# Kernel tuning notes

Hardware: AMD Instinct MI355X
Metric: run time of the kernel (lower is better)

## Reference

```python
import jax, jax.numpy as jnp
import numpy as np
import math

NUM_CLASSES = 80
ANCHORS = [(12.0, 16.0), (19.0, 36.0), (40.0, 28.0)]
ANGLES = [-np.pi/3, -np.pi/6, 0.0, np.pi/6, np.pi/3, np.pi/2]
STRIDE = 8.0
SCALE_XY = 1.05
IGNORE_THRESH = 0.5
MASKED_ANCHORS = np.array([[w/STRIDE, h/STRIDE, a] for (w, h) in ANCHORS for a in ANGLES], dtype=np.float32)  # [18,3]
NA = MASKED_ANCHORS.shape[0]
LAMBDA_COORD, LAMBDA_CONF, LAMBDA_CLS = 1.0, 10.0, 1.0
FOCAL_ALPHA, FOCAL_GAMMA = 0.25, 2.0


def setup_inputs() -> dict:
    key = jax.random.key(0)
    B, G, nT = 8, 76, 240
    k1, k2, k3, k4, k5, k6 = jax.random.split(key, 6)
    output = jax.random.normal(k1, (B, NA * (NUM_CLASSES + 6), G, G), jnp.float32) * 0.1
    tb = jax.random.randint(k2, (nT,), 0, B).astype(jnp.float32)
    tl = jax.random.randint(k3, (nT,), 0, NUM_CLASSES).astype(jnp.float32)
    txy = jax.random.uniform(k4, (nT, 2), minval=0.02, maxval=0.98)
    twh = jax.random.uniform(k5, (nT, 2), minval=0.05, maxval=0.4)
    tang = jax.random.uniform(k6, (nT, 1), minval=-np.pi/2, maxval=np.pi/2)
    target = jnp.concatenate([tb[:, None], tl[:, None], txy, twh, tang], axis=-1)  # [nT,7]
    return {"output": output, "target": target}


def _smooth_l1(x, y):
    d = jnp.abs(x - y)
    return jnp.where(d < 1.0, 0.5 * d * d, d - 0.5)


def _bce(p, t):
    eps = 1e-7
    p = jnp.clip(p, eps, 1.0 - eps)
    return -(t * jnp.log(p) + (1.0 - t) * jnp.log(1.0 - p))


def _focal(p, t):
    loss = _bce(p, t)
    p_t = t * p + (1.0 - t) * (1.0 - p)
    alpha_f = t * FOCAL_ALPHA + (1.0 - t) * (1.0 - FOCAL_ALPHA)
    return loss * alpha_f * (1.0 - p_t) ** FOCAL_GAMMA


def _ciou(pb, tb):
    # pb, tb: [N,5] (cx, cy, w, h, angle) in grid units
    p1, p2 = pb[:, :2] - pb[:, 2:4] / 2, pb[:, :2] + pb[:, 2:4] / 2
    t1, t2 = tb[:, :2] - tb[:, 2:4] / 2, tb[:, :2] + tb[:, 2:4] / 2
    w1, h1 = p2[:, 0] - p1[:, 0], p2[:, 1] - p1[:, 1]
    w2, h2 = t2[:, 0] - t1[:, 0], t2[:, 1] - t1[:, 1]
    area1, area2 = w1 * h1, w2 * h2
    c1, c2 = (p1 + p2) / 2, (t1 + t2) / 2
    inter = jnp.clip(jnp.minimum(p2, t2) - jnp.maximum(p1, t1), 0.0)
    inter_area = inter[:, 0] * inter[:, 1]
    inter_diag = jnp.sum((c2 - c1) ** 2, axis=-1)
    outer = jnp.clip(jnp.maximum(p2, t2) - jnp.minimum(p1, t1), 0.0)
    outer_diag = outer[:, 0] ** 2 + outer[:, 1] ** 2
    union = area1 + area2 - inter_area
    u = inter_diag / outer_diag
    iou = inter_area / union
    v = (4.0 / math.pi ** 2) * (jnp.arctan(w2 / h2) - jnp.arctan(w1 / h1)) ** 2
    alpha = jax.lax.stop_gradient(v / ((1.0 - iou) + v))
    ciou = jnp.clip(iou - (u + alpha * v), -1.0, 1.0)
    skew_iou = iou * jnp.abs(jnp.cos(pb[:, 4] - tb[:, 4]))
    return skew_iou, ciou


def _forward(output, target):
    B, G = output.shape[0], output.shape[2]
    nC = NUM_CLASSES
    ma = jnp.asarray(MASKED_ANCHORS)
    pred = output.reshape(B, NA, nC + 6, G, G).transpose(0, 1, 3, 4, 2)  # [B,A,G,G,C+6]
    px = jax.nn.sigmoid(pred[..., 0]) * SCALE_XY - (SCALE_XY - 1) / 2
    py = jax.nn.sigmoid(pred[..., 1]) * SCALE_XY - (SCALE_XY - 1) / 2
    pw, ph, pa = pred[..., 2], pred[..., 3], pred[..., 4]
    pconf = jax.nn.sigmoid(pred[..., 5])
    pcls = jax.nn.sigmoid(pred[..., 6:])
    gx = jnp.arange(G, dtype=output.dtype)[None, None, None, :]
    gy = jnp.arange(G, dtype=output.dtype)[None, None, :, None]
    aw = ma[:, 0].reshape(1, NA, 1, 1)
    ah = ma[:, 1].reshape(1, NA, 1, 1)
    aa = ma[:, 2].reshape(1, NA, 1, 1)
    pred_boxes = jnp.stack([px + gx, py + gy, jnp.exp(pw) * aw, jnp.exp(ph) * ah, pa + aa], axis=-1)  # [B,A,G,G,5]
    out_dec = jnp.concatenate([
        jnp.concatenate([pred_boxes[..., :4] * STRIDE, pred_boxes[..., 4:]], axis=-1).reshape(B, -1, 5),
        pconf.reshape(B, -1, 1),
        pcls.reshape(B, -1, nC)], axis=-1)

    # ---- build_targets ----
    tgt_boxes = jnp.concatenate([target[:, 2:6] * G, target[:, 6:]], axis=-1)  # [nT,5]
    gxy, gwh, ga = tgt_boxes[:, :2], tgt_boxes[:, 2:4], tgt_boxes[:, 4]
    aw_, ah_, aa_ = ma[:, 0][:, None], ma[:, 1][:, None], ma[:, 2][:, None]  # [A,1]
    w2, h2 = gwh[:, 0][None, :], gwh[:, 1][None, :]                          # [1,nT]
    inter = jnp.minimum(aw_, w2) * jnp.minimum(ah_, h2)
    union = aw_ * ah_ + 1e-16 + w2 * h2 - inter
    offset = jnp.abs(aa_ - ga[None, :])                                       # [A,nT]
    arious = (inter / union) * jnp.abs(jnp.cos(aa_ - ga[None, :]))            # [A,nT]
    best_n = jnp.argmax(arious, axis=0)                                       # [nT]
    b = target[:, 0].astype(jnp.int32)
    labels = target[:, 1].astype(jnp.int32)
    gi = gxy[:, 0].astype(jnp.int32)
    gj = gxy[:, 1].astype(jnp.int32)

    zeros = jnp.zeros((B, NA, G, G), output.dtype)
    obj = zeros.at[b, best_n, gj, gi].set(1.0)
    noobj = jnp.ones((B, NA, G, G), output.dtype)
    cond = (arious > IGNORE_THRESH) | ((arious > 0.4) & (offset < np.pi / 12))  # [A,nT]
    a_idx = jnp.broadcast_to(jnp.arange(NA)[:, None], arious.shape)
    bb = jnp.broadcast_to(b[None, :], arious.shape)
    gjb = jnp.broadcast_to(gj[None, :], arious.shape)
    gib = jnp.broadcast_to(gi[None, :], arious.shape)
    noobj = noobj.at[bb, a_idx, gjb, gib].min(jnp.where(cond, 0.0, 1.0))
    noobj = noobj.at[b, best_n, gj, gi].set(0.0)

    ta_grid = zeros.at[b, best_n, gj, gi].set(ga - ma[best_n, 2])
    tcls = jnp.zeros((B, NA, G, G, nC), output.dtype).at[b, best_n, gj, gi, labels].set(1.0)
    tconf = obj

    pb = pred_boxes[b, best_n, gj, gi]  # [nT,5]
    iou, ciou = _ciou(pb, tgt_boxes)
    img_size = STRIDE * G
    bbox_scale = jax.lax.stop_gradient(2.0 - gwh[:, 0] * gwh[:, 1] / img_size ** 2)
    ciou_t = bbox_scale * (1.0 - ciou)

    class_ok = (jnp.argmax(pcls[b, best_n, gj, gi], axis=-1) == labels).astype(output.dtype)
    class_mask = zeros.at[b, best_n, gj, gi].set(class_ok)
    iou_scores = zeros.at[b, best_n, gj, gi].set(iou)
    skew = zeros.at[b, best_n, gj, gi].set(jnp.exp(1.0 - iou) - 1.0)
    ciou_grid = zeros.at[b, best_n, gj, gi].set(ciou_t)

    # ---- losses (masked means replace boolean indexing) ----
    n_obj = jnp.maximum(jnp.sum(obj), 1.0)
    n_noobj = jnp.maximum(jnp.sum(noobj), 1.0)
    reg = _smooth_l1(pa, ta_grid) + ciou_grid
    reg_const = jax.lax.stop_gradient(skew / jnp.where(obj > 0, reg, 1.0))
    reg_loss = jnp.sum(reg * reg_const * obj) / n_obj
    fl = _focal(pconf, tconf)
    conf_loss = jnp.sum(fl * obj) / n_obj + jnp.sum(fl * noobj) / n_noobj
    cls_loss = jnp.sum(_bce(pcls, tcls) * obj[..., None]) / (n_obj * nC)
    total_loss = LAMBDA_COORD * reg_loss + LAMBDA_CONF * conf_loss + LAMBDA_CLS * cls_loss
    return out_dec, total_loss


def reference(output, target):
    return _forward(output, target)
```

## Files before the change

kernel.cpp:

```cpp
#include <hip/hip_runtime.h>
#include <math.h>

#define NCLS 80
#define NANC 18
#define NB 8
#define GG 76
#define SS (GG*GG)
#define CHN (NCLS+6)
#define NCELL (NB*NANC*SS)
#define FLAG_WORDS ((NCELL+31)/32)
#define NT_MAX 240
#define TILE 76
#define LSTR 77
#define TPB 4
#define TGRP (GG/TPB)
#define THR 256
#define NLOAD 7
#define TOT4 (CHN*(TILE/4))
#define NTRANS (NB*NANC*TGRP)
#define NCONF4 (NCELL/4)
#define NCONFBLK ((NCONF4+255)/256)
#define PI_ 3.14159265358979323846

#define WS_WIN   64
#define WS_META  1024
#define WS_LM    4864
#define WS_FLAGS 6784

typedef float fx4 __attribute__((ext_vector_type(4)));
typedef float fx2 __attribute__((ext_vector_type(2)));

__device__ __constant__ float d_ma[NANC][3] = {
  {1.5f, 2.0f, (float)(-PI_/3)}, {1.5f, 2.0f, (float)(-PI_/6)}, {1.5f, 2.0f, 0.0f},
  {1.5f, 2.0f, (float)(PI_/6)},  {1.5f, 2.0f, (float)(PI_/3)},  {1.5f, 2.0f, (float)(PI_/2)},
  {2.375f, 4.5f, (float)(-PI_/3)}, {2.375f, 4.5f, (float)(-PI_/6)}, {2.375f, 4.5f, 0.0f},
  {2.375f, 4.5f, (float)(PI_/6)},  {2.375f, 4.5f, (float)(PI_/3)},  {2.375f, 4.5f, (float)(PI_/2)},
  {5.0f, 3.5f, (float)(-PI_/3)}, {5.0f, 3.5f, (float)(-PI_/6)}, {5.0f, 3.5f, 0.0f},
  {5.0f, 3.5f, (float)(PI_/6)},  {5.0f, 3.5f, (float)(PI_/3)},  {5.0f, 3.5f, (float)(PI_/2)},
};

__device__ __forceinline__ float sigm(float x) { return 1.0f / (1.0f + expf(-x)); }
__device__ __forceinline__ float fsig(float x) {
  return __builtin_amdgcn_rcpf(1.0f + __expf(-x));
}

__global__ __launch_bounds__(256) void k_prep(const float* __restrict__ tgt,
                                              unsigned* __restrict__ flags,
                                              int* __restrict__ win,
                                              int4* __restrict__ meta,
                                              uint2* __restrict__ lmout,
                                              int* __restrict__ cnt,
                                              double* __restrict__ acc, int nT) {
  __shared__ int s_key[NT_MAX], s_lab[NT_MAX];
  __shared__ int s_win[NT_MAX];
  __shared__ int s_zero;

  int t = threadIdx.x;
  uint4* f4 = (uint4*)flags;
  for (int i = t; i < FLAG_WORDS/4; i += 256) f4[i] = make_uint4(0,0,0,0);
  if (t < 4) { acc[t] = 0.0; cnt[t] = 0; }
  if (t == 0) s_zero = 0;
  __syncthreads();

  int bi = 0, gi = 0, gj = 0, bn = 0;
  unsigned cm = 0;
  if (t < nT) {
    float bf = tgt[t*7+0], lf = tgt[t*7+1];
    float gx = tgt[t*7+2] * (float)GG, gy = tgt[t*7+3] * (float)GG;
    float gw = tgt[t*7+4] * (float)GG, gh = tgt[t*7+5] * (float)GG;
    float ga = tgt[t*7+6];
    bi = (int)bf; gi = (int)gx; gj = (int)gy;
    int lab = (int)lf;
    float best = -1e30f;
    for (int a = 0; a < NANC; ++a) {
      float aw = d_ma[a][0], ah = d_ma[a][1], aa = d_ma[a][2];
      float inter = fminf(aw, gw) * fminf(ah, gh);
      float uni = aw*ah + 1e-16f + gw*gh - inter;
      float off = fabsf(aa - ga);
      float ar = inter / uni * fabsf(cosf(aa - ga));
      if (ar > best) { best = ar; bn = a; }
      if (ar > 0.5f || (ar > 0.4f && off < (float)(PI_/12))) cm |= (1u << a);
    }
    s_key[t] = ((bi*NANC + bn)*GG + gj)*GG + gi;
    s_lab[t] = lab;
    s_win[t] = 0;
  }
  __syncthreads();

  if (t < nT) {
    for (int a = 0; a < NANC; ++a) {
      if (((cm >> a) & 1u) || a == bn) {
        int cell = ((bi*NANC + a)*GG + gj)*GG + gi;
        unsigned bit = 1u << (cell & 31);
        unsigned old = atomicOr(&flags[cell >> 5], bit);
        if (!(old & bit)) atomicAdd(&s_zero, 1);
      }
    }
    int key = s_key[t];
    bool winner = true;
    for (int t2 = t + 1; t2 < nT; ++t2) if (s_key[t2] == key) { winner = false; break; }
    if (winner) {
      s_win[t] = 1;
      unsigned long long lm0 = 0, lm1 = 0;
      for (int t2 = 0; t2 < nT; ++t2) if (s_key[t2] == key) {
        int L = s_lab[t2];
        if (L < 64) lm0 |= 1ull << L; else lm1 |= 1ull << (L - 64);
      }
      lmout[t] = make_uint2((unsigned)(lm0 & 0xffffffffull), (unsigned)(lm0 >> 32));
      meta[t] = make_int4(bi, bn, gi, gj | ((int)(lm1 & 0xffffu) << 16));
      win[t] = 1;
    } else {
      win[t] = 0;
    }
  }
  __syncthreads();
  if (t == 0) {
    int nw = 0;
    for (int i = 0; i < nT; ++i) nw += s_win[i];
    cnt[0] = s_zero; cnt[1] = nw;
  }
}

__global__ __launch_bounds__(THR) void k_fused(const float* __restrict__ in,
                                               float* __restrict__ out,
                                               const unsigned* __restrict__ flags,
                                               const float* __restrict__ tgt,
                                               const int* __restrict__ win,
                                               const int4* __restrict__ meta,
                                               const uint2* __restrict__ lm,
                                               double* __restrict__ acc,
                                               int* __restrict__ cnt,
                                               int nT) {
  __shared__ float lds[CHN * LSTR];
  int nloss = nT + NCONFBLK;
  int blk = blockIdx.x;
  int tid = threadIdx.x;

  if (blk < nloss) {
    if (blk < nT) {
      if (win[blk]) {
        int t = blk;
        int4 m = meta[t];
        int bi = m.x, bn = m.y, gi = m.z, gj = m.w & 0xffff;
        unsigned lmhi = ((unsigned)m.w) >> 16;
        uint2 l0 = lm[t];
        const float* base = in + ((size_t)(bi*NANC + bn)*CHN)*SS + (size_t)gj*GG + gi;

        float csum = 0.0f;
        if (tid < NCLS) {
          float p = fsig(base[(size_t)(6 + tid)*SS]);
          float pl = fminf(fmaxf(p, 1e-7f), 1.0f - 1e-7f);
          bool tc;
          if (tid < 32)      tc = (l0.x >> tid) & 1u;
          else if (tid < 64) tc = (l0.y >> (tid - 32)) & 1u;
          else               tc = (lmhi >> (tid - 64)) & 1u;
          csum = tc ? -__logf(pl) : -__logf(1.0f - pl);
        }
        for (int off = 32; off; off >>= 1) csum += __shfl_down(csum, off);
        if ((tid & 63) == 0 && tid < 128) atomicAdd(&acc[3], (double)csum);

        if (tid == 128) {
          float gx = tgt[t*7+2] * (float)GG, gyv = tgt[t*7+3] * (float)GG;
          float gw = tgt[t*7+4] * (float)GG, gh = tgt[t*7+5] * (float)GG;
          float ga = tgt[t*7+6];
          float rx = base[0], ry = base[(size_t)SS], rw = base[2*(size_t)SS],
                rh = base[3*(size_t)SS], ra = base[4*(size_t)SS], rcf = base[5*(size_t)SS];
          float aw = d_ma[bn][0], ah = d_ma[bn][1], aa = d_ma[bn][2];
          float px = sigm(rx)*1.05f - 0.025f + (float)gi;
          float py = sigm(ry)*1.05f - 0.025f + (float)gj;
          float pw = expf(rw)*aw, ph = expf(rh)*ah;
          float pang = ra + aa;
          float p1x = px - pw*0.5f, p1y = py - ph*0.5f, p2x = px + pw*0.5f, p2y = py + ph*0.5f;
          float t1x = gx - gw*0.5f, t1y = gyv - gh*0.5f, t2x = gx + gw*0.5f, t2y = gyv + gh*0.5f;
          float w1 = p2x - p1x, h1 = p2y - p1y, w2 = t2x - t1x, h2 = t2y - t1y;
          float area1 = w1*h1, area2 = w2*h2;
          float c1x = (p1x+p2x)*0.5f, c1y = (p1y+p2y)*0.5f, c2x = (t1x+t2x)*0.5f, c2y = (t1y+t2y)*0.5f;
          float ix = fmaxf(fminf(p2x,t2x) - fmaxf(p1x,t1x), 0.0f);
          float iy = fmaxf(fminf(p2y,t2y) - fmaxf(p1y,t1y), 0.0f);
          float inter_area = ix*iy;
          float dcx = c2x - c1x, dcy = c2y - c1y;
          float inter_diag = dcx*dcx + dcy*dcy;
          float ox = fmaxf(fmaxf(p2x,t2x) - fminf(p1x,t1x), 0.0f);
          float oy = fmaxf(fmaxf(p2y,t2y) - fminf(p1y,t1y), 0.0f);
          float outer_diag = ox*ox + oy*oy;
          float uni = area1 + area2 - inter_area;
          float u = inter_diag / outer_diag;
          float iou = inter_area / uni;
          float da = atanf(w2/h2) - atanf(w1/h1);
          float v = (float)(4.0/(PI_*PI_)) * da * da;
          float alpha = v / (1.0f - iou + v);
          float ciou = fminf(fmaxf(iou - (u + alpha*v), -1.0f), 1.0f);
          float skew_iou = iou * fabsf(cosf(pang - ga));
          float skew = expf(1.0f - skew_iou) - 1.0f;
          float bscale = 2.0f - gw*gh/369664.0f;
          float ciou_t = bscale * (1.0f - ciou);
          float ta = ga - aa;
          float d = fabsf(ra - ta);
          float sl1 = (d < 1.0f) ? 0.5f*d*d : d - 0.5f;
          float reg = sl1 + ciou_t;
          atomicAdd(&acc[2], (double)(reg * (skew / reg)));
          float pc = sigm(rcf);
          float pcl = fminf(fmaxf(pc, 1e-7f), 1.0f - 1e-7f);
          float om = 1.0f - pc;
          atomicAdd(&acc[1], (double)(-logf(pcl) * 0.25f * om * om));
        }
      }
    } else {
      __shared__ double wsum[4];
      int j = (blk - nT)*256 + tid;
      double fl = 0.0;
      if (j < NCONF4) {
        int ba = j / (SS/4);
        int q  = j - ba*(SS/4);
        int spos = 4*q;
        const float4 v4 = *(const float4*)(in + (size_t)ba*CHN*SS + 5*(size_t)SS + spos);
        int cell0 = ba*SS + spos;
        unsigned word = flags[cell0 >> 5];
        int bbit = cell0 & 31;
        float pv[4] = {v4.x, v4.y, v4.z, v4.w};
        #pragma unroll
        for (int e = 0; e < 4; ++e) {
          if (!((word >> (bbit + e)) & 1u)) {
            float p = fsig(pv[e]);
            float pcl = fminf(fmaxf(p, 1e-7f), 1.0f - 1e-7f);
            fl += (double)(-__logf(1.0f - pcl) * 0.75f * p * p);
          }
        }
      }
      int lane = tid & 63, wid = tid >> 6;
      for (int off = 32; off; off >>= 1) fl += __shfl_down(fl, off);
      if (lane == 0) wsum[wid] = fl;
      __syncthreads();
      if (tid == 0) {
        double s = wsum[0] + wsum[1] + wsum[2] + wsum[3];
        if (s != 0.0) atomicAdd(&acc[0], s);
      }
    }
    __syncthreads();
    if (tid == 0) {
      __threadfence();
      unsigned tk = atomicAdd((unsigned*)&cnt[2], 1u);
      if (tk == (unsigned)(nloss - 1)) {
        double a0 = atomicAdd(&acc[0], 0.0);
        double a1 = atomicAdd(&acc[1], 0.0);
        double a2 = atomicAdd(&acc[2], 0.0);
        double a3 = atomicAdd(&acc[3], 0.0);
        int c0 = atomicAdd(&cnt[0], 0);
        int c1 = atomicAdd(&cnt[1], 0);
        double n_obj = fmax((double)c1, 1.0);
        double n_noobj = fmax((double)(NCELL - c0), 1.0);
        double loss = a2/n_obj + 10.0*(a1/n_obj + a0/n_noobj) + a3/(n_obj*(double)NCLS);
        out[(size_t)NCELL*CHN] = (float)loss;
      }
    }
    return;
  }

  int tblk = blk - nloss;
  int tgrp = tblk % TGRP;
  int ba = tblk / TGRP;
  int a = ba % NANC;
  float aw8 = d_ma[a][0]*8.0f, ah8 = d_ma[a][1]*8.0f, aa = d_ma[a][2];
  const float* plane_in = in + (size_t)ba*CHN*SS;
  float* plane_out = out + (size_t)ba*SS*CHN;
  int tile0 = tgrp*TPB;

  float4 r[NLOAD];
  { const float* tin = plane_in + tile0*TILE;
    #pragma unroll
    for (int k = 0; k < NLOAD; ++k) {
      int i = threadIdx.x + k*THR;
      if (i < TOT4) { int c = i/19, s4 = i - c*19;
        r[k] = *(const float4*)(tin + (size_t)c*SS + 4*s4); } }
  }

  for (int tt = 0; tt < TPB; ++tt) {
    int tile = tile0 + tt;
    __syncthreads();
    #pragma unroll
    for (int k = 0; k < NLOAD; ++k) {
      int i = threadIdx.x + k*THR;
      if (i < TOT4) {
        int c = i/19, s4 = i - c*19;
        float* p = &lds[c*LSTR + 4*s4];
        p[0] = r[k].x; p[1] = r[k].y; p[2] = r[k].z; p[3] = r[k].w;
      }
    }
    __syncthreads();
    if (tt + 1 < TPB) {
      const float* tin = plane_in + (tile + 1)*TILE;
      #pragma unroll
      for (int k = 0; k < NLOAD; ++k) {
        int i = threadIdx.x + k*THR;
        if (i < TOT4) { int c = i/19, s4 = i - c*19;
          r[k] = *(const float4*)(tin + (size_t)c*SS + 4*s4); } }
    }
    float gyf = (float)tile;
    float* orow = plane_out + (size_t)tile*TILE*CHN;
    for (int q = threadIdx.x; q < TILE*22; q += THR) {
      int s = q / 22;
      int j = q - s*22;
      int par = s & 1;
      if (j < 21) {
        int c = 2*par + 4*j;
        float v0 = lds[(c  )*LSTR + s];
        float v1 = lds[(c+1)*LSTR + s];
        float v2 = lds[(c+2)*LSTR + s];
        float v3 = lds[(c+3)*LSTR + s];
        fx4 R;
        if (c >= 6) {
          R.x = fsig(v0); R.y = fsig(v1); R.z = fsig(v2); R.w = fsig(v3);
        } else if (c == 0) {
          R.x = (fsig(v0)*1.05f - 0.025f + (float)s)*8.0f;
          R.y = (fsig(v1)*1.05f - 0.025f + gyf)*8.0f;
          R.z = __expf(v2)*aw8;
          R.w = __expf(v3)*ah8;
        } else if (c == 4) {
          R.x = v0 + aa;
          R.y = fsig(v1);
          R.z = fsig(v2);
          R.w = fsig(v3);
        } else {
          R.x = __expf(v0)*aw8;
          R.y = __expf(v1)*ah8;
          R.z = v2 + aa;
          R.w = fsig(v3);
        }
        __builtin_nontemporal_store(R, (fx4*)(orow + s*CHN + c));
      } else {
        int c = par ? 0 : 84;
        float v0 = lds[(c  )*LSTR + s];
        float v1 = lds[(c+1)*LSTR + s];
        fx2 R;
        if (par) {
          R.x = (fsig(v0)*1.05f - 0.025f + (float)s)*8.0f;
          R.y = (fsig(v1)*1.05f - 0.025f + gyf)*8.0f;
        } else {
          R.x = fsig(v0); R.y = fsig(v1);
        }
        __builtin_nontemporal_store(R, (fx2*)(orow + s*CHN + c));
      }
    }
  }
}

extern "C" void kernel_launch(void* const* d_in, const int* in_sizes, int n_in,
                              void* d_out, int out_size, void* d_ws, size_t ws_size,
                              hipStream_t stream) {
  const float* in  = (const float*)d_in[0];
  const float* tgt = (const float*)d_in[1];
  float* out = (float*)d_out;
  double* acc = (double*)d_ws;
  int* cnt = (int*)((char*)d_ws + 32);
  int* win = (int*)((char*)d_ws + WS_WIN);
  int4* meta = (int4*)((char*)d_ws + WS_META);
  uint2* lm = (uint2*)((char*)d_ws + WS_LM);
  unsigned* flags = (unsigned*)((char*)d_ws + WS_FLAGS);
  int nT = in_sizes[1] / 7;
  if (nT > NT_MAX) nT = NT_MAX;

  hipLaunchKernelGGL(k_prep, dim3(1), dim3(256), 0, stream,
                     tgt, flags, win, meta, lm, cnt, acc, nT);
  hipLaunchKernelGGL(k_fused, dim3(nT + NCONFBLK + NTRANS), dim3(THR), 0, stream,
                     in, out, flags, tgt, win, meta, lm, acc, cnt, nT);
}
```

Measured before the change: 223.5 us.

## Move workspace zeroing into a parallel kernel and drop nontemporal output stores

Zeroing of the flag bitmap and the accumulators moves out of the single-block prep kernel into a separate multi-block k_zero kernel, so the clears run across many workgroups instead of one. The decoded output stores switch from nontemporal builtins to plain float4/float2 stores. The change adds an extra kernel launch, and regular stores may behave differently in cache than the nontemporal path.

```diff
diff --git a/kernel.cpp b/kernel.cpp
--- a/kernel.cpp
+++ b/kernel.cpp
@@ -20,15 +20,13 @@
 #define NTRANS (NB*NANC*TGRP)
 #define NCONF4 (NCELL/4)
 #define NCONFBLK ((NCONF4+255)/256)
+#define ZWORDS (16 + FLAG_WORDS)
 #define PI_ 3.14159265358979323846
 
 #define WS_WIN   64
 #define WS_META  1024
 #define WS_LM    4864
 #define WS_FLAGS 6784
-
-typedef float fx4 __attribute__((ext_vector_type(4)));
-typedef float fx2 __attribute__((ext_vector_type(2)));
 
 __device__ __constant__ float d_ma[NANC][3] = {
   {1.5f, 2.0f, (float)(-PI_/3)}, {1.5f, 2.0f, (float)(-PI_/6)}, {1.5f, 2.0f, 0.0f},
@@ -44,21 +42,23 @@
   return __builtin_amdgcn_rcpf(1.0f + __expf(-x));
 }
 
+__global__ void k_zero(unsigned* __restrict__ ws_words, unsigned* __restrict__ flags) {
+  int i = blockIdx.x * blockDim.x + threadIdx.x;
+  if (i < 16) ws_words[i] = 0u;
+  if (i < FLAG_WORDS) flags[i] = 0u;
+}
+
 __global__ __launch_bounds__(256) void k_prep(const float* __restrict__ tgt,
                                               unsigned* __restrict__ flags,
                                               int* __restrict__ win,
                                               int4* __restrict__ meta,
                                               uint2* __restrict__ lmout,
-                                              int* __restrict__ cnt,
-                                              double* __restrict__ acc, int nT) {
+                                              int* __restrict__ cnt, int nT) {
   __shared__ int s_key[NT_MAX], s_lab[NT_MAX];
   __shared__ int s_win[NT_MAX];
   __shared__ int s_zero;
 
   int t = threadIdx.x;
-  uint4* f4 = (uint4*)flags;
-  for (int i = t; i < FLAG_WORDS/4; i += 256) f4[i] = make_uint4(0,0,0,0);
-  if (t < 4) { acc[t] = 0.0; cnt[t] = 0; }
   if (t == 0) s_zero = 0;
   __syncthreads();
 
@@ -307,9 +307,9 @@
         float v1 = lds[(c+1)*LSTR + s];
         float v2 = lds[(c+2)*LSTR + s];
         float v3 = lds[(c+3)*LSTR + s];
-        fx4 R;
+        float4 R;
         if (c >= 6) {
-          R.x = fsig(v0); R.y = fsig(v1); R.z = fsig(v2); R.w = fsig(v3);
+          R = make_float4(fsig(v0), fsig(v1), fsig(v2), fsig(v3));
         } else if (c == 0) {
           R.x = (fsig(v0)*1.05f - 0.025f + (float)s)*8.0f;
           R.y = (fsig(v1)*1.05f - 0.025f + gyf)*8.0f;
@@ -326,19 +326,19 @@
           R.z = v2 + aa;
           R.w = fsig(v3);
         }
-        __builtin_nontemporal_store(R, (fx4*)(orow + s*CHN + c));
+        *(float4*)(orow + s*CHN + c) = R;
       } else {
         int c = par ? 0 : 84;
         float v0 = lds[(c  )*LSTR + s];
         float v1 = lds[(c+1)*LSTR + s];
-        fx2 R;
+        float2 R;
         if (par) {
           R.x = (fsig(v0)*1.05f - 0.025f + (float)s)*8.0f;
           R.y = (fsig(v1)*1.05f - 0.025f + gyf)*8.0f;
         } else {
-          R.x = fsig(v0); R.y = fsig(v1);
-        }
-        __builtin_nontemporal_store(R, (fx2*)(orow + s*CHN + c));
+          R = make_float2(fsig(v0), fsig(v1));
+        }
+        *(float2*)(orow + s*CHN + c) = R;
       }
     }
   }
@@ -359,8 +359,10 @@
   int nT = in_sizes[1] / 7;
   if (nT > NT_MAX) nT = NT_MAX;
 
+  hipLaunchKernelGGL(k_zero, dim3((FLAG_WORDS + 255)/256), dim3(256), 0, stream,
+                     (unsigned*)d_ws, flags);
   hipLaunchKernelGGL(k_prep, dim3(1), dim3(256), 0, stream,
-                     tgt, flags, win, meta, lm, cnt, acc, nT);
+                     tgt, flags, win, meta, lm, cnt, nT);
   hipLaunchKernelGGL(k_fused, dim3(nT + NCONFBLK + NTRANS), dim3(THR), 0, stream,
                      in, out, flags, tgt, win, meta, lm, acc, cnt, nT);
 }
```

After: 235.2 us. 1.05x slower.
